# Optimization experiments

Measured on AMD Instinct MI355X. Metric: run time of the kernel, lower is better.

The kernel has to match this reference:

```python
import jax, jax.numpy as jnp
import numpy as np

ALPHA = 1.5
N_ITER = 100
TOL = 1e-5


def _gp(x, alpha):
    return (x ** (alpha - 1.0) - 1.0) / (alpha - 1.0)


def _gp_inv(y, alpha):
    return (1.0 + (alpha - 1.0) * y) ** (1.0 / (alpha - 1.0))


def _p(X, min_val, alpha):
    # clamp then invert the generalized log (gp)
    return _gp_inv(jnp.maximum(X, min_val), alpha)


def tsallis_secant(X, alpha=ALPHA, n_iter=N_ITER, tol=TOL):
    # X: [..., d]; secant root-finding for the entmax threshold tau along last dim
    d = X.shape[-1]
    gp_zero = _gp(0.0, alpha)  # = -1/(alpha-1) for alpha>1 (0**(a-1)=0)
    max_val = X.max(axis=-1)
    lo = max_val - _gp(1.0, alpha)
    hi = max_val - _gp(1.0 / d, alpha)
    p_lo = _p(X - lo[..., None], gp_zero, alpha)
    p_hi = _p(X - hi[..., None], gp_zero, alpha)
    f_lo = p_lo.sum(axis=-1) - 1.0
    f_hi = p_hi.sum(axis=-1) - 1.0

    def body(it, carry):
        lo, hi, f_lo, f_hi, p_hi = carry
        mask = (f_lo - f_hi) ** 2 >= tol  # rows still unconverged
        denom = jnp.where(mask, f_hi - f_lo, 1.0)  # avoid NaN on converged rows
        tau = (lo * f_hi - hi * f_lo) / denom
        new_lo = hi
        new_hi = jnp.where(mask, tau, hi)
        p_new = _p(X - new_hi[..., None], gp_zero, alpha)
        new_p_hi = jnp.where(mask[..., None], p_new, p_hi)
        new_f_lo = f_hi
        new_f_hi = new_p_hi.sum(axis=-1) - 1.0
        return (new_lo, new_hi, new_f_lo, new_f_hi, new_p_hi)

    carry = jax.lax.fori_loop(0, n_iter, body, (lo, hi, f_lo, f_hi, p_hi))
    return carry[4]


def setup_inputs() -> dict:
    key = jax.random.key(0)
    X = jax.random.normal(key, (4096, 32000), dtype=jnp.float32)
    return {"X": X}


def reference(X):
    return tsallis_secant(X, ALPHA, N_ITER, TOL)
```

## Files before the change

kernel.cpp:

```cpp
#include <hip/hip_runtime.h>

#define D        32000
#define DV       8000
#define BLOCK    512
#define NWAVES   (BLOCK / 64)
#define NCHUNK   16
#define FULLC    15
#define TAILLIM  320

__device__ __forceinline__ float wave_reduce_sum(float v) {
    v += __shfl_xor(v, 32, 64);
    v += __shfl_xor(v, 16, 64);
    v += __shfl_xor(v,  8, 64);
    v += __shfl_xor(v,  4, 64);
    v += __shfl_xor(v,  2, 64);
    v += __shfl_xor(v,  1, 64);
    return v;
}

__device__ __forceinline__ float wave_reduce_max(float v) {
    v = fmaxf(v, __shfl_xor(v, 32, 64));
    v = fmaxf(v, __shfl_xor(v, 16, 64));
    v = fmaxf(v, __shfl_xor(v,  8, 64));
    v = fmaxf(v, __shfl_xor(v,  4, 64));
    v = fmaxf(v, __shfl_xor(v,  2, 64));
    v = fmaxf(v, __shfl_xor(v,  1, 64));
    return v;
}

__global__ __launch_bounds__(BLOCK, 4) void tsallis_secant_kernel(
        const float* __restrict__ X, float* __restrict__ out) {
    const int row  = blockIdx.x;
    const int tid  = threadIdx.x;
    const int wave = tid >> 6;
    const int lane = tid & 63;

    __shared__ float sbuf[2][NWAVES];

    const float4* __restrict__ Xv = (const float4*)(X + (size_t)row * D);
    float4* __restrict__ Ov       = (float4*)(out + (size_t)row * D);

    float4 u[NCHUNK];
    float m = -1e30f;
#pragma unroll
    for (int i = 0; i < NCHUNK; ++i) {
        if (i < FULLC || tid < TAILLIM) {
            float4 x = Xv[i * BLOCK + tid];
            float4 uu;
            uu.x = fmaf(0.5f, x.x, 1.0f);
            uu.y = fmaf(0.5f, x.y, 1.0f);
            uu.z = fmaf(0.5f, x.z, 1.0f);
            uu.w = fmaf(0.5f, x.w, 1.0f);
            u[i] = uu;
            m = fmaxf(m, fmaxf(fmaxf(uu.x, uu.y), fmaxf(uu.z, uu.w)));
        } else {
            u[i] = make_float4(-1e30f, -1e30f, -1e30f, -1e30f);
        }
    }

    m = wave_reduce_max(m);
    if (lane == 0) sbuf[0][wave] = m;
    __syncthreads();
    float umax = sbuf[0][0];
#pragma unroll
    for (int w = 1; w < NWAVES; ++w) umax = fmaxf(umax, sbuf[0][w]);
    __syncthreads();

    float t_lo = umax - 1.0f;
    float t_hi = umax - 0.00559016994f;

    int parity = 0;

    auto feval = [&](float t) -> float {
        float a0 = 0.f, a1 = 0.f, a2 = 0.f, a3 = 0.f;
#pragma unroll
        for (int i = 0; i < NCHUNK; ++i) {
            float v;
            v = fmaxf(u[i].x - t, 0.f); a0 = fmaf(v, v, a0);
            v = fmaxf(u[i].y - t, 0.f); a1 = fmaf(v, v, a1);
            v = fmaxf(u[i].z - t, 0.f); a2 = fmaf(v, v, a2);
            v = fmaxf(u[i].w - t, 0.f); a3 = fmaf(v, v, a3);
        }
        float s = wave_reduce_sum((a0 + a1) + (a2 + a3));
        if (lane == 0) sbuf[parity][wave] = s;
        __syncthreads();
        float f = sbuf[parity][0];
#pragma unroll
        for (int w = 1; w < NWAVES; ++w) f += sbuf[parity][w];
        parity ^= 1;
        return f - 1.0f;
    };

    float f_lo = feval(t_lo);
    float f_hi = feval(t_hi);

    for (int it = 0; it < 100; ++it) {
        float diff = f_lo - f_hi;
        if (diff * diff < 1e-5f) break;
        float t_new = (t_lo * f_hi - t_hi * f_lo) / (f_hi - f_lo);
        t_lo = t_hi;
        f_lo = f_hi;
        t_hi = t_new;
        f_hi = feval(t_hi);
    }

    const float t = t_hi;
#pragma unroll
    for (int i = 0; i < NCHUNK; ++i) {
        if (i < FULLC || tid < TAILLIM) {
            float4 p; float v;
            v = fmaxf(u[i].x - t, 0.f); p.x = v * v;
            v = fmaxf(u[i].y - t, 0.f); p.y = v * v;
            v = fmaxf(u[i].z - t, 0.f); p.z = v * v;
            v = fmaxf(u[i].w - t, 0.f); p.w = v * v;
            Ov[i * BLOCK + tid] = p;
        }
    }
}

extern "C" void kernel_launch(void* const* d_in, const int* in_sizes, int n_in,
                              void* d_out, int out_size, void* d_ws, size_t ws_size,
                              hipStream_t stream) {
    const float* X = (const float*)d_in[0];
    float* out     = (float*)d_out;
    const int rows = in_sizes[0] / D;
    tsallis_secant_kernel<<<rows, BLOCK, 0, stream>>>(X, out);
}
```

Baseline: 825.3 us.

## Compact candidate support into shared list for secant iterations

After finding the row max, each thread counts the elements above xmax-2 (the only ones that can be nonzero once tau >= umax-1). It compacts them into a shared-memory list of up to 2048 entries. Secant evaluations then sum over at most four values per thread instead of 64. The code falls back to the full scan if the list overflows or tau drops below the floor. This adds an atomic, extra barriers and shared memory, which may lower occupancy.

```diff
diff --git a/kernel.cpp b/kernel.cpp
--- a/kernel.cpp
+++ b/kernel.cpp
@@ -1,12 +1,15 @@
 #include <hip/hip_runtime.h>
 
 #define D        32000
-#define DV       8000
 #define BLOCK    512
 #define NWAVES   (BLOCK / 64)
 #define NCHUNK   16
 #define FULLC    15
 #define TAILLIM  320
+#define CAP      2048
+#define CPT      (CAP / BLOCK)
+
+#define NEGBIG   -1e30f
 
 __device__ __forceinline__ float wave_reduce_sum(float v) {
     v += __shfl_xor(v, 32, 64);
@@ -36,60 +39,109 @@
     const int lane = tid & 63;
 
     __shared__ float sbuf[2][NWAVES];
+    __shared__ float list[CAP];
+    __shared__ int   s_cnt;
+    __shared__ float s_max;
 
     const float4* __restrict__ Xv = (const float4*)(X + (size_t)row * D);
     float4* __restrict__ Ov       = (float4*)(out + (size_t)row * D);
 
-    float4 u[NCHUNK];
-    float m = -1e30f;
+    if (tid == 0) s_cnt = 0;
+
+    float4 x[NCHUNK];
+    float mx = NEGBIG;
 #pragma unroll
     for (int i = 0; i < NCHUNK; ++i) {
         if (i < FULLC || tid < TAILLIM) {
-            float4 x = Xv[i * BLOCK + tid];
-            float4 uu;
-            uu.x = fmaf(0.5f, x.x, 1.0f);
-            uu.y = fmaf(0.5f, x.y, 1.0f);
-            uu.z = fmaf(0.5f, x.z, 1.0f);
-            uu.w = fmaf(0.5f, x.w, 1.0f);
-            u[i] = uu;
-            m = fmaxf(m, fmaxf(fmaxf(uu.x, uu.y), fmaxf(uu.z, uu.w)));
+            float4 xv = Xv[i * BLOCK + tid];
+            x[i] = xv;
+            mx = fmaxf(mx, fmaxf(fmaxf(xv.x, xv.y), fmaxf(xv.z, xv.w)));
         } else {
-            u[i] = make_float4(-1e30f, -1e30f, -1e30f, -1e30f);
+            x[i] = make_float4(NEGBIG, NEGBIG, NEGBIG, NEGBIG);
         }
     }
 
-    m = wave_reduce_max(m);
-    if (lane == 0) sbuf[0][wave] = m;
+    mx = wave_reduce_max(mx);
+    if (lane == 0) sbuf[0][wave] = mx;
     __syncthreads();
-    float umax = sbuf[0][0];
+    float xmax = sbuf[0][0];
 #pragma unroll
-    for (int w = 1; w < NWAVES; ++w) umax = fmaxf(umax, sbuf[0][w]);
+    for (int w = 1; w < NWAVES; ++w) xmax = fmaxf(xmax, sbuf[0][w]);
+
+    const float umax    = fmaf(0.5f, xmax, 1.0f);
+    const float t_floor = umax - 1.0f;
+    const float xcut    = xmax - 2.0f;
+
+    int nloc = 0;
+#pragma unroll
+    for (int i = 0; i < NCHUNK; ++i) {
+        nloc += (x[i].x > xcut) + (x[i].y > xcut) +
+                (x[i].z > xcut) + (x[i].w > xcut);
+    }
     __syncthreads();
+    int base = (nloc > 0) ? atomicAdd(&s_cnt, nloc) : 0;
+#pragma unroll
+    for (int i = 0; i < NCHUNK; ++i) {
+        float xs[4] = {x[i].x, x[i].y, x[i].z, x[i].w};
+#pragma unroll
+        for (int k = 0; k < 4; ++k) {
+            if (xs[k] > xcut) {
+                if (base < CAP) list[base] = fmaf(0.5f, xs[k], 1.0f);
+                ++base;
+            }
+        }
+    }
+    __syncthreads();
+    const int  cnt = s_cnt;
+    const bool ok  = (cnt <= CAP);
 
-    float t_lo = umax - 1.0f;
-    float t_hi = umax - 0.00559016994f;
+    float c[CPT];
+#pragma unroll
+    for (int k = 0; k < CPT; ++k) {
+        int idx = tid + k * BLOCK;
+        c[k] = (idx < cnt) ? list[idx] : NEGBIG;
+    }
 
     int parity = 0;
-
-    auto feval = [&](float t) -> float {
-        float a0 = 0.f, a1 = 0.f, a2 = 0.f, a3 = 0.f;
-#pragma unroll
-        for (int i = 0; i < NCHUNK; ++i) {
-            float v;
-            v = fmaxf(u[i].x - t, 0.f); a0 = fmaf(v, v, a0);
-            v = fmaxf(u[i].y - t, 0.f); a1 = fmaf(v, v, a1);
-            v = fmaxf(u[i].z - t, 0.f); a2 = fmaf(v, v, a2);
-            v = fmaxf(u[i].w - t, 0.f); a3 = fmaf(v, v, a3);
-        }
-        float s = wave_reduce_sum((a0 + a1) + (a2 + a3));
+    auto block_sum = [&](float partial) -> float {
+        float s = wave_reduce_sum(partial);
         if (lane == 0) sbuf[parity][wave] = s;
         __syncthreads();
         float f = sbuf[parity][0];
 #pragma unroll
         for (int w = 1; w < NWAVES; ++w) f += sbuf[parity][w];
         parity ^= 1;
-        return f - 1.0f;
+        return f;
     };
+
+    auto feval_fast = [&](float t) -> float {
+        float a = 0.f;
+#pragma unroll
+        for (int k = 0; k < CPT; ++k) {
+            float v = fmaxf(c[k] - t, 0.f);
+            a = fmaf(v, v, a);
+        }
+        return block_sum(a) - 1.0f;
+    };
+    auto feval_full = [&](float t) -> float {
+        const float omt = 1.0f - t;
+        float a0 = 0.f, a1 = 0.f, a2 = 0.f, a3 = 0.f;
+#pragma unroll
+        for (int i = 0; i < NCHUNK; ++i) {
+            float v;
+            v = fmaxf(fmaf(0.5f, x[i].x, omt), 0.f); a0 = fmaf(v, v, a0);
+            v = fmaxf(fmaf(0.5f, x[i].y, omt), 0.f); a1 = fmaf(v, v, a1);
+            v = fmaxf(fmaf(0.5f, x[i].z, omt), 0.f); a2 = fmaf(v, v, a2);
+            v = fmaxf(fmaf(0.5f, x[i].w, omt), 0.f); a3 = fmaf(v, v, a3);
+        }
+        return block_sum((a0 + a1) + (a2 + a3)) - 1.0f;
+    };
+    auto feval = [&](float t) -> float {
+        return (ok && t >= t_floor) ? feval_fast(t) : feval_full(t);
+    };
+
+    float t_lo = t_floor;
+    float t_hi = umax - 0.00559016994f;
 
     float f_lo = feval(t_lo);
     float f_hi = feval(t_hi);
@@ -104,15 +156,15 @@
         f_hi = feval(t_hi);
     }
 
-    const float t = t_hi;
+    const float omt = 1.0f - t_hi;
 #pragma unroll
     for (int i = 0; i < NCHUNK; ++i) {
         if (i < FULLC || tid < TAILLIM) {
             float4 p; float v;
-            v = fmaxf(u[i].x - t, 0.f); p.x = v * v;
-            v = fmaxf(u[i].y - t, 0.f); p.y = v * v;
-            v = fmaxf(u[i].z - t, 0.f); p.z = v * v;
-            v = fmaxf(u[i].w - t, 0.f); p.w = v * v;
+            v = fmaxf(fmaf(0.5f, x[i].x, omt), 0.f); p.x = v * v;
+            v = fmaxf(fmaf(0.5f, x[i].y, omt), 0.f); p.y = v * v;
+            v = fmaxf(fmaf(0.5f, x[i].z, omt), 0.f); p.z = v * v;
+            v = fmaxf(fmaf(0.5f, x[i].w, omt), 0.f); p.w = v * v;
             Ov[i * BLOCK + tid] = p;
         }
     }
```

New measurement: 823.3 us. No clear change (-0.2%).
